# Performance work log

Measured on AMD Instinct MI355X. Metric: run time of the kernel, lower is better.

Reference implementation:

```python
import jax, jax.numpy as jnp
import numpy as np
from jax import lax

STRIDE, PAD, K = 1, 1, 3


def conv2d(x, w, b, stride, pad):
    y = lax.conv_general_dilated(x, w, (stride, stride), [(pad, pad), (pad, pad)],
                                 dimension_numbers=('NCHW', 'OIHW', 'NCHW'))
    return y + b[None, :, None, None]


def deform_conv2d(x, offset, mask, weight, stride, pad):
    # torchvision DeformConv2d v2 (modulated): offset channels are (dy, dx) pairs per tap.
    B, C, H, W = x.shape
    O = weight.shape[0]
    K2 = K * K
    Ho = (H + 2 * pad - K) // stride + 1
    Wo = (W + 2 * pad - K) // stride + 1
    off = offset.reshape(B, K2, 2, Ho, Wo)
    dy, dx = off[:, :, 0], off[:, :, 1]                      # [B,K2,Ho,Wo]
    ki = (jnp.arange(K2) // K).astype(x.dtype)[None, :, None, None]
    kj = (jnp.arange(K2) % K).astype(x.dtype)[None, :, None, None]
    hg = (jnp.arange(Ho) * stride - pad).astype(x.dtype)[None, None, :, None]
    wg = (jnp.arange(Wo) * stride - pad).astype(x.dtype)[None, None, None, :]
    py = hg + ki + dy                                        # sampling y coord [B,K2,Ho,Wo]
    px = wg + kj + dx
    y0 = jnp.floor(py)
    x0 = jnp.floor(px)
    ly = py - y0
    lx = px - x0
    y0i = y0.astype(jnp.int32)
    x0i = x0.astype(jnp.int32)
    x_flat = x.reshape(B, C, H * W)

    def gather(iy, ix):
        valid = ((iy >= 0) & (iy < H) & (ix >= 0) & (ix < W)).astype(x.dtype)
        idx = jnp.clip(iy, 0, H - 1) * W + jnp.clip(ix, 0, W - 1)   # [B,K2,Ho,Wo]
        v = jax.vmap(lambda xf, id_: xf[:, id_])(x_flat, idx)       # [B,C,K2,Ho,Wo]
        return v * valid[:, None]

    v = ((1 - ly) * (1 - lx))[:, None] * gather(y0i, x0i) \
      + ((1 - ly) * lx)[:, None] * gather(y0i, x0i + 1) \
      + (ly * (1 - lx))[:, None] * gather(y0i + 1, x0i) \
      + (ly * lx)[:, None] * gather(y0i + 1, x0i + 1)
    v = v * mask[:, None]                                    # modulate per tap
    return jnp.einsum('bckhw,ock->bohw', v, weight.reshape(O, C, K2))


def setup_inputs():
    key = jax.random.key(0)
    ks = jax.random.split(key, 5)
    B, C, H, W, O = 4, 64, 96, 96, 128
    x = jax.random.normal(ks[0], (B, C, H, W), jnp.float32)
    offset_w = jax.random.normal(ks[1], (2 * K * K, C, K, K), jnp.float32) * 0.01
    offset_b = jax.random.normal(ks[2], (2 * K * K,), jnp.float32) * 0.1
    mod_w = jax.random.normal(ks[3], (K * K, C, K, K), jnp.float32) * 0.01
    mod_b = jnp.zeros((K * K,), jnp.float32)
    deform_w = jax.random.normal(ks[4], (O, C, K, K), jnp.float32) * (1.0 / np.sqrt(C * K * K))
    return {"x": x, "offset_w": offset_w, "offset_b": offset_b,
            "mod_w": mod_w, "mod_b": mod_b, "deform_w": deform_w}


def reference(x, offset_w, offset_b, mod_w, mod_b, deform_w):
    offset = conv2d(x, offset_w, offset_b, STRIDE, PAD)
    modulator = 2.0 * jax.nn.sigmoid(conv2d(x, mod_w, mod_b, STRIDE, PAD))
    return deform_conv2d(x, offset, modulator, deform_w, STRIDE, PAD)
```

## Files before the change

kernel.cpp:

```cpp
#include <hip/hip_runtime.h>
#include <math.h>

#define Bc 4
#define Cc 64
#define Hh 96
#define Ww 96
#define Oo 128
#define HW 9216
#define PT 32
#define NPB 288
#define RW 34
#define RS 72

typedef __attribute__((ext_vector_type(8))) short bf16x8;
typedef __attribute__((ext_vector_type(4))) float f32x4;

__device__ inline unsigned short f2bf(float f) {
    unsigned u = __builtin_bit_cast(unsigned, f);
    return (unsigned short)((u + 0x7FFF + ((u >> 16) & 1)) >> 16);
}
__device__ inline float bf2f(short s) {
    return __builtin_bit_cast(float, ((unsigned)(unsigned short)s) << 16);
}

__global__ __launch_bounds__(256) void k_pre(
    const float* __restrict__ dw, const float* __restrict__ ow,
    const float* __restrict__ mw, const float* __restrict__ x,
    unsigned short* __restrict__ wTmF, unsigned short* __restrict__ w27F,
    unsigned short* __restrict__ xT)
{
    const int bid = blockIdx.x;
    const int t = threadIdx.x;
    if (bid < 360) {
        int i = bid * 256 + t;
        if (i < 9 * 8 * 2 * 512) {
            int j = i & 7, l = (i >> 3) & 63, fb = i >> 9;
            int s = fb & 1, m = (fb >> 1) & 7, k = fb >> 4;
            int oc = m * 16 + (l & 15);
            int c = s * 32 + (l >> 4) * 8 + j;
            wTmF[i] = f2bf(dw[(oc * 64 + c) * 9 + k]);
        }
        int jj = i - 9 * 8 * 2 * 512;
        if (jj >= 0 && jj < 9 * 2 * 2 * 512) {
            int j = jj & 7, l = (jj >> 3) & 63, fb2 = jj >> 9;
            int nt = fb2 & 1, s = (fb2 >> 1) & 1, k = fb2 >> 2;
            int ch = nt * 16 + (l & 15);
            int c = s * 32 + (l >> 4) * 8 + j;
            float v = 0.f;
            if (ch < 18)      v = ow[(ch * 64 + c) * 9 + k];
            else if (ch < 27) v = mw[((ch - 18) * 64 + c) * 9 + k];
            w27F[jj] = f2bf(v);
        }
    } else {
        int gp = (bid - 360) * 256 + t;
        int b = gp / HW;
        int p = gp - b * HW;
        const float* xb = x + (size_t)b * Cc * HW + p;
        unsigned short* op = xT + (size_t)gp * 64;
#pragma unroll
        for (int q = 0; q < 8; ++q) {
            union { bf16x8 v8; unsigned short us[8]; } u;
#pragma unroll
            for (int c = 0; c < 8; ++c)
                u.us[c] = f2bf(xb[(size_t)(q * 8 + c) * HW]);
            *(bf16x8*)(op + q * 8) = u.v8;
        }
    }
}

__global__ __launch_bounds__(256, 6) void k_fused(
    const unsigned short* __restrict__ xT, const float* __restrict__ ob,
    const float* __restrict__ mb, const unsigned short* __restrict__ w27F,
    const unsigned short* __restrict__ wTmF, float* __restrict__ out)
{
    __shared__ union Ovl {
        short xreg[3 * RW * RS];
        struct {
            float pw[9][4][PT];
            int   pi[9][4][PT];
        } p;
    } ovl;
    __shared__ float offm_s[27 * 33];

    const int t = threadIdx.x;
    const int lid = (blockIdx.x & 7) * 144 + (blockIdx.x >> 3);
    const int bb = lid / NPB;
    const int tile = lid - bb * NPB;
    const int ho = tile / 3;
    const int wo0 = (tile - ho * 3) * 32;
    const int wv = t >> 6;
    const int l = t & 63;
    const int lr = l & 15;
    const int quad = l >> 4;

    const unsigned short* xTb = xT + (size_t)bb * HW * 64;

    static const bf16x8 zero8 = {0, 0, 0, 0, 0, 0, 0, 0};
    for (int i = t; i < 3 * RW * 8; i += 256) {
        int q = i & 7;
        int rc = i >> 3;
        int col = rc % RW, r = rc / RW;
        int h = ho + r - 1, w = wo0 + col - 1;
        bf16x8 val = zero8;
        if ((unsigned)h < (unsigned)Hh && (unsigned)w < (unsigned)Ww)
            val = *(const bf16x8*)(xTb + ((size_t)(h * Ww + w)) * 64 + q * 8);
        *(bf16x8*)&ovl.xreg[(r * RW + col) * RS + q * 8] = val;
    }
    __syncthreads();

    {
        f32x4 acc_o = {0.f, 0.f, 0.f, 0.f};
        const int mt1 = wv & 1;
        const int nt1 = wv >> 1;
#pragma unroll
        for (int k9 = 0; k9 < 9; ++k9) {
            const int di = k9 / 3, dj = k9 % 3;
            const short* ar = &ovl.xreg[(di * RW + mt1 * 16 + lr + dj) * RS + quad * 8];
#pragma unroll
            for (int s = 0; s < 2; ++s) {
                bf16x8 a = *(const bf16x8*)(ar + s * 32);
                bf16x8 b = *(const bf16x8*)(w27F + (((k9 * 2 + s) * 2 + nt1) << 9) + l * 8);
                acc_o = __builtin_amdgcn_mfma_f32_16x16x32_bf16(a, b, acc_o, 0, 0, 0);
            }
        }
        __syncthreads();
        int ch = nt1 * 16 + lr;
        if (ch < 27) {
#pragma unroll
            for (int r = 0; r < 4; ++r)
                offm_s[ch * 33 + mt1 * 16 + quad * 4 + r] = acc_o[r];
        }
    }
    __syncthreads();

    for (int i = t; i < 27 * PT; i += 256) {
        int ch = i >> 5, pos = i & 31;
        float v = offm_s[ch * 33 + pos];
        if (ch < 18) v += ob[ch];
        else         v = 2.f / (1.f + expf(-(v + mb[ch - 18])));
        offm_s[ch * 33 + pos] = v;
    }
    __syncthreads();
    for (int i = t; i < 9 * PT; i += 256) {
        int kk = i >> 5, pos = i & 31;
        float dy = offm_s[(2 * kk) * 33 + pos];
        float dx = offm_s[(2 * kk + 1) * 33 + pos];
        float mm = offm_s[(18 + kk) * 33 + pos];
        float py = (float)(ho - 1 + kk / 3) + dy;
        float px = (float)(wo0 + pos - 1 + kk % 3) + dx;
        float fy = floorf(py), fx = floorf(px);
        float ly = py - fy, lx = px - fx;
        int y0 = (int)fy, x0 = (int)fx;
        int y1 = y0 + 1, x1 = x0 + 1;
        float v00 = ((unsigned)y0 < (unsigned)Hh && (unsigned)x0 < (unsigned)Ww) ? 1.f : 0.f;
        float v01 = ((unsigned)y0 < (unsigned)Hh && (unsigned)x1 < (unsigned)Ww) ? 1.f : 0.f;
        float v10 = ((unsigned)y1 < (unsigned)Hh && (unsigned)x0 < (unsigned)Ww) ? 1.f : 0.f;
        float v11 = ((unsigned)y1 < (unsigned)Hh && (unsigned)x1 < (unsigned)Ww) ? 1.f : 0.f;
        int cy0 = min(max(y0, 0), Hh - 1), cy1 = min(max(y1, 0), Hh - 1);
        int cx0 = min(max(x0, 0), Ww - 1), cx1 = min(max(x1, 0), Ww - 1);
        ovl.p.pw[kk][0][pos] = (1.f - ly) * (1.f - lx) * mm * v00;
        ovl.p.pw[kk][1][pos] = (1.f - ly) * lx * mm * v01;
        ovl.p.pw[kk][2][pos] = ly * (1.f - lx) * mm * v10;
        ovl.p.pw[kk][3][pos] = ly * lx * mm * v11;
        ovl.p.pi[kk][0][pos] = (cy0 * Ww + cx0) * 64;
        ovl.p.pi[kk][1][pos] = (cy0 * Ww + cx1) * 64;
        ovl.p.pi[kk][2][pos] = (cy1 * Ww + cx0) * 64;
        ovl.p.pi[kk][3][pos] = (cy1 * Ww + cx1) * 64;
    }
    __syncthreads();

    const int mh = wv >> 1;
    const int nt = wv & 1;
    const int pos_l = nt * 16 + lr;
    const int cq = quad * 8;

    f32x4 acc[4];
#pragma unroll
    for (int m = 0; m < 4; ++m) acc[m] = (f32x4){0.f, 0.f, 0.f, 0.f};

    const unsigned short* wb = wTmF + l * 8;

    bf16x8 curC[4], nxtC[4];
#pragma unroll
    for (int cr = 0; cr < 4; ++cr)
        curC[cr] = *(const bf16x8*)(xTb + ovl.p.pi[0][cr][pos_l] + cq);

#pragma unroll
    for (int k9 = 0; k9 < 9; ++k9) {
        const float w0 = ovl.p.pw[k9][0][pos_l], w1 = ovl.p.pw[k9][1][pos_l];
        const float w2 = ovl.p.pw[k9][2][pos_l], w3 = ovl.p.pw[k9][3][pos_l];

#pragma unroll
        for (int cr = 0; cr < 4; ++cr)
            nxtC[cr] = *(const bf16x8*)(xTb + ovl.p.pi[k9][cr][pos_l] + 32 + cq);
        {
            union { bf16x8 v8; unsigned short us[8]; } B;
#pragma unroll
            for (int j = 0; j < 8; ++j) {
                float v = w0 * bf2f(curC[0][j]) + w1 * bf2f(curC[1][j])
                        + w2 * bf2f(curC[2][j]) + w3 * bf2f(curC[3][j]);
                B.us[j] = f2bf(v);
            }
#pragma unroll
            for (int m = 0; m < 4; ++m) {
                bf16x8 A = *(const bf16x8*)(
                    wb + (size_t)((k9 * 16 + (mh * 4 + m) * 2 + 0) << 9));
                acc[m] = __builtin_amdgcn_mfma_f32_16x16x32_bf16(A, B.v8, acc[m], 0, 0, 0);
            }
        }

        if (k9 < 8) {
#pragma unroll
            for (int cr = 0; cr < 4; ++cr)
                curC[cr] = *(const bf16x8*)(xTb + ovl.p.pi[k9 + 1][cr][pos_l] + cq);
        }
        {
            union { bf16x8 v8; unsigned short us[8]; } B;
#pragma unroll
            for (int j = 0; j < 8; ++j) {
                float v = w0 * bf2f(nxtC[0][j]) + w1 * bf2f(nxtC[1][j])
                        + w2 * bf2f(nxtC[2][j]) + w3 * bf2f(nxtC[3][j]);
                B.us[j] = f2bf(v);
            }
#pragma unroll
            for (int m = 0; m < 4; ++m) {
                bf16x8 A = *(const bf16x8*)(
                    wb + (size_t)((k9 * 16 + (mh * 4 + m) * 2 + 1) << 9));
                acc[m] = __builtin_amdgcn_mfma_f32_16x16x32_bf16(A, B.v8, acc[m], 0, 0, 0);
            }
        }
    }

    float* outp = out + (size_t)bb * Oo * HW + tile * PT + nt * 16 + lr;
#pragma unroll
    for (int m = 0; m < 4; ++m) {
#pragma unroll
        for (int r = 0; r < 4; ++r) {
            int oc = mh * 64 + m * 16 + quad * 4 + r;
            outp[(size_t)oc * HW] = acc[m][r];
        }
    }
}

extern "C" void kernel_launch(void* const* d_in, const int* in_sizes, int n_in,
                              void* d_out, int out_size, void* d_ws, size_t ws_size,
                              hipStream_t stream) {
    const float* x  = (const float*)d_in[0];
    const float* ow = (const float*)d_in[1];
    const float* ob = (const float*)d_in[2];
    const float* mw = (const float*)d_in[3];
    const float* mb = (const float*)d_in[4];
    const float* dw = (const float*)d_in[5];
    float* out = (float*)d_out;

    unsigned short* wTmF = (unsigned short*)d_ws;
    unsigned short* w27F = wTmF + 9 * 8 * 2 * 512;
    unsigned short* xT   = w27F + 9 * 2 * 2 * 512;

    hipLaunchKernelGGL(k_pre, dim3(504), dim3(256), 0, stream,
                       dw, ow, mw, x, wTmF, w27F, xT);
    hipLaunchKernelGGL(k_fused, dim3(Bc * NPB), dim3(256), 0, stream,
                       xT, ob, mb, w27F, wTmF, out);
}
```

Baseline: 131.9 us.

## Split deformable conv taps across wave groups instead of output channels

Waves previously split output channels in halves, so each wave bilinearly sampled all 9 taps. Now each wave computes all 128 output channels (8 accumulators) over a subset of taps (0-4 or 5-8), and partial sums are reduced through LDS before the store. This halves the redundant gather and interpolation work per block. In exchange it adds an LDS reduction, two extra barriers and a load imbalance between the 5-tap and 4-tap wave groups. It also doubles accumulator registers, lowering launch bounds occupancy from 6 to 4.

```diff
diff --git a/kernel.cpp b/kernel.cpp
--- a/kernel.cpp
+++ b/kernel.cpp
@@ -68,7 +68,60 @@
     }
 }
 
-__global__ __launch_bounds__(256, 6) void k_fused(
+template <int K0, int K1>
+__device__ __forceinline__ void sample_gemm(
+    const unsigned short* __restrict__ xTb,
+    const unsigned short* __restrict__ wb,
+    const float (&pw)[9][4][PT], const int (&pi)[9][4][PT],
+    int pos_l, int cq, f32x4 (&acc)[8])
+{
+    bf16x8 curC[4], nxtC[4];
+#pragma unroll
+    for (int cr = 0; cr < 4; ++cr)
+        curC[cr] = *(const bf16x8*)(xTb + pi[K0][cr][pos_l] + cq);
+
+#pragma unroll
+    for (int k9 = K0; k9 < K1; ++k9) {
+        const float w0 = pw[k9][0][pos_l], w1 = pw[k9][1][pos_l];
+        const float w2 = pw[k9][2][pos_l], w3 = pw[k9][3][pos_l];
+
+#pragma unroll
+        for (int cr = 0; cr < 4; ++cr)
+            nxtC[cr] = *(const bf16x8*)(xTb + pi[k9][cr][pos_l] + 32 + cq);
+        {
+            union { bf16x8 v8; unsigned short us[8]; } B;
+#pragma unroll
+            for (int j = 0; j < 8; ++j)
+                B.us[j] = f2bf(w0 * bf2f(curC[0][j]) + w1 * bf2f(curC[1][j])
+                             + w2 * bf2f(curC[2][j]) + w3 * bf2f(curC[3][j]));
+#pragma unroll
+            for (int m = 0; m < 8; ++m) {
+                bf16x8 A = *(const bf16x8*)(wb + (size_t)((k9 * 16 + m * 2 + 0) << 9));
+                acc[m] = __builtin_amdgcn_mfma_f32_16x16x32_bf16(A, B.v8, acc[m], 0, 0, 0);
+            }
+        }
+
+        if (k9 + 1 < K1) {
+#pragma unroll
+            for (int cr = 0; cr < 4; ++cr)
+                curC[cr] = *(const bf16x8*)(xTb + pi[k9 + 1][cr][pos_l] + cq);
+        }
+        {
+            union { bf16x8 v8; unsigned short us[8]; } B;
+#pragma unroll
+            for (int j = 0; j < 8; ++j)
+                B.us[j] = f2bf(w0 * bf2f(nxtC[0][j]) + w1 * bf2f(nxtC[1][j])
+                             + w2 * bf2f(nxtC[2][j]) + w3 * bf2f(nxtC[3][j]));
+#pragma unroll
+            for (int m = 0; m < 8; ++m) {
+                bf16x8 A = *(const bf16x8*)(wb + (size_t)((k9 * 16 + m * 2 + 1) << 9));
+                acc[m] = __builtin_amdgcn_mfma_f32_16x16x32_bf16(A, B.v8, acc[m], 0, 0, 0);
+            }
+        }
+    }
+}
+
+__global__ __launch_bounds__(256, 4) void k_fused(
     const unsigned short* __restrict__ xT, const float* __restrict__ ob,
     const float* __restrict__ mb, const unsigned short* __restrict__ w27F,
     const unsigned short* __restrict__ wTmF, float* __restrict__ out)
@@ -79,6 +132,7 @@
             float pw[9][4][PT];
             int   pi[9][4][PT];
         } p;
+        float mg[8 * 520];
     } ovl;
     __shared__ float offm_s[27 * 33];
 
@@ -169,75 +223,39 @@
     }
     __syncthreads();
 
-    const int mh = wv >> 1;
     const int nt = wv & 1;
+    const int tg = wv >> 1;
     const int pos_l = nt * 16 + lr;
     const int cq = quad * 8;
 
-    f32x4 acc[4];
-#pragma unroll
-    for (int m = 0; m < 4; ++m) acc[m] = (f32x4){0.f, 0.f, 0.f, 0.f};
+    f32x4 acc[8];
+#pragma unroll
+    for (int m = 0; m < 8; ++m) acc[m] = (f32x4){0.f, 0.f, 0.f, 0.f};
 
     const unsigned short* wb = wTmF + l * 8;
 
-    bf16x8 curC[4], nxtC[4];
-#pragma unroll
-    for (int cr = 0; cr < 4; ++cr)
-        curC[cr] = *(const bf16x8*)(xTb + ovl.p.pi[0][cr][pos_l] + cq);
-
-#pragma unroll
-    for (int k9 = 0; k9 < 9; ++k9) {
-        const float w0 = ovl.p.pw[k9][0][pos_l], w1 = ovl.p.pw[k9][1][pos_l];
-        const float w2 = ovl.p.pw[k9][2][pos_l], w3 = ovl.p.pw[k9][3][pos_l];
-
-#pragma unroll
-        for (int cr = 0; cr < 4; ++cr)
-            nxtC[cr] = *(const bf16x8*)(xTb + ovl.p.pi[k9][cr][pos_l] + 32 + cq);
-        {
-            union { bf16x8 v8; unsigned short us[8]; } B;
-#pragma unroll
-            for (int j = 0; j < 8; ++j) {
-                float v = w0 * bf2f(curC[0][j]) + w1 * bf2f(curC[1][j])
-                        + w2 * bf2f(curC[2][j]) + w3 * bf2f(curC[3][j]);
-                B.us[j] = f2bf(v);
-            }
-#pragma unroll
-            for (int m = 0; m < 4; ++m) {
-                bf16x8 A = *(const bf16x8*)(
-                    wb + (size_t)((k9 * 16 + (mh * 4 + m) * 2 + 0) << 9));
-                acc[m] = __builtin_amdgcn_mfma_f32_16x16x32_bf16(A, B.v8, acc[m], 0, 0, 0);
-            }
-        }
-
-        if (k9 < 8) {
-#pragma unroll
-            for (int cr = 0; cr < 4; ++cr)
-                curC[cr] = *(const bf16x8*)(xTb + ovl.p.pi[k9 + 1][cr][pos_l] + cq);
-        }
-        {
-            union { bf16x8 v8; unsigned short us[8]; } B;
-#pragma unroll
-            for (int j = 0; j < 8; ++j) {
-                float v = w0 * bf2f(nxtC[0][j]) + w1 * bf2f(nxtC[1][j])
-                        + w2 * bf2f(nxtC[2][j]) + w3 * bf2f(nxtC[3][j]);
-                B.us[j] = f2bf(v);
-            }
-#pragma unroll
-            for (int m = 0; m < 4; ++m) {
-                bf16x8 A = *(const bf16x8*)(
-                    wb + (size_t)((k9 * 16 + (mh * 4 + m) * 2 + 1) << 9));
-                acc[m] = __builtin_amdgcn_mfma_f32_16x16x32_bf16(A, B.v8, acc[m], 0, 0, 0);
-            }
-        }
-    }
-
-    float* outp = out + (size_t)bb * Oo * HW + tile * PT + nt * 16 + lr;
-#pragma unroll
-    for (int m = 0; m < 4; ++m) {
-#pragma unroll
-        for (int r = 0; r < 4; ++r) {
-            int oc = mh * 64 + m * 16 + quad * 4 + r;
-            outp[(size_t)oc * HW] = acc[m][r];
+    if (tg == 0)
+        sample_gemm<0, 5>(xTb, wb, ovl.p.pw, ovl.p.pi, pos_l, cq, acc);
+    else
+        sample_gemm<5, 9>(xTb, wb, ovl.p.pw, ovl.p.pi, pos_l, cq, acc);
+
+    __syncthreads();
+    if (tg == 1) {
+#pragma unroll
+        for (int m = 0; m < 8; ++m)
+            *(f32x4*)&ovl.mg[m * 520 + (nt * 64 + l) * 4] = acc[m];
+    }
+    __syncthreads();
+    if (tg == 0) {
+        float* outp = out + (size_t)bb * Oo * HW + tile * PT + nt * 16 + lr;
+#pragma unroll
+        for (int m = 0; m < 8; ++m) {
+            f32x4 o = acc[m] + *(const f32x4*)&ovl.mg[m * 520 + (nt * 64 + l) * 4];
+#pragma unroll
+            for (int r = 0; r < 4; ++r) {
+                int oc = m * 16 + quad * 4 + r;
+                outp[(size_t)oc * HW] = o[r];
+            }
         }
     }
 }
```

New measurement: 116.1 us. 12.0% less time.
